# Kernel optimization log

Hardware: AMD Instinct MI355X
Metric: run time of the kernel (lower is better)

The kernel has to match this reference:

```python
import jax, jax.numpy as jnp
import numpy as np

H = 20  # hidden_size

def _lstm_layer(x_tbf, w_ih, w_hh, b_ih, b_hh):
    # x_tbf: [T, B, F]; torch gate order: i, f, g, o
    T, B, _ = x_tbf.shape
    # precompute input projections once: [T, B, 4H]
    xproj = jnp.einsum('tbf,gf->tbg', x_tbf, w_ih) + b_ih + b_hh

    def step(carry, xp_t):
        h, c = carry
        gates = xp_t + h @ w_hh.T  # [B, 4H]
        i, f, g, o = jnp.split(gates, 4, axis=-1)
        i = jax.nn.sigmoid(i)
        f = jax.nn.sigmoid(f)
        g = jnp.tanh(g)
        o = jax.nn.sigmoid(o)
        c = f * c + i * g
        h = o * jnp.tanh(c)
        return (h, c), h

    h0 = jnp.zeros((B, H), dtype=x_tbf.dtype)
    c0 = jnp.zeros((B, H), dtype=x_tbf.dtype)
    (_, _), hs = jax.lax.scan(step, (h0, c0), xproj)
    return hs  # [T, B, H]

def setup_inputs() -> dict:
    key = jax.random.key(0)
    ks = jax.random.split(key, 11)
    F_in = 10
    s_ih0 = 1.0 / np.sqrt(H)
    inp = {
        'x': jax.random.normal(ks[0], (4096, 512, F_in), dtype=jnp.float32),
        'w_ih0': jax.random.uniform(ks[1], (4 * H, F_in), minval=-s_ih0, maxval=s_ih0),
        'w_hh0': jax.random.uniform(ks[2], (4 * H, H), minval=-s_ih0, maxval=s_ih0),
        'b_ih0': jax.random.uniform(ks[3], (4 * H,), minval=-s_ih0, maxval=s_ih0),
        'b_hh0': jax.random.uniform(ks[4], (4 * H,), minval=-s_ih0, maxval=s_ih0),
        'w_ih1': jax.random.uniform(ks[5], (4 * H, H), minval=-s_ih0, maxval=s_ih0),
        'w_hh1': jax.random.uniform(ks[6], (4 * H, H), minval=-s_ih0, maxval=s_ih0),
        'b_ih1': jax.random.uniform(ks[7], (4 * H,), minval=-s_ih0, maxval=s_ih0),
        'b_hh1': jax.random.uniform(ks[8], (4 * H,), minval=-s_ih0, maxval=s_ih0),
        'w_fc': jax.random.uniform(ks[9], (1, H), minval=-s_ih0, maxval=s_ih0),
        'b_fc': jax.random.uniform(ks[10], (1,), minval=-s_ih0, maxval=s_ih0),
    }
    return inp

def reference(x, w_ih0, w_hh0, b_ih0, b_hh0, w_ih1, w_hh1, b_ih1, b_hh1, w_fc, b_fc):
    # x: [B, T, F] (batch_first) -> [T, B, F] for scan
    x_tbf = jnp.swapaxes(x, 0, 1)
    h1 = _lstm_layer(x_tbf, w_ih0, w_hh0, b_ih0, b_hh0)  # [T, B, H]
    h2 = _lstm_layer(h1, w_ih1, w_hh1, b_ih1, b_hh1)     # [T, B, H]
    last = h2[-1]                                          # [B, H]
    return last @ w_fc.T + b_fc                            # [B, 1]
```

## Files before the change

### kernel.cpp

```cpp
#include <hip/hip_runtime.h>

#define T_STEPS 512
#define HS 20
#define F0 10
#define BPB 6
#define NB_TOT 4096
#define NBLK ((NB_TOT + BPB - 1) / BPB)

__device__ __forceinline__ float sigmoid_fast(float v) {
    return __fdividef(1.f, 1.f + __expf(-v));
}
__device__ __forceinline__ float tanh_fast(float v) {
    return 1.f - __fdividef(2.f, __expf(2.f * v) + 1.f);
}
#define PIN(v) asm volatile("" : "+v"(v))

__global__ __launch_bounds__(256, 3)
void lstm2_fc_kernel(const float* __restrict__ x,
                     const float* __restrict__ wih0, const float* __restrict__ whh0,
                     const float* __restrict__ bih0, const float* __restrict__ bhh0,
                     const float* __restrict__ wih1, const float* __restrict__ whh1,
                     const float* __restrict__ bih1, const float* __restrict__ bhh1,
                     const float* __restrict__ wfc,  const float* __restrict__ bfc,
                     float* __restrict__ out)
{
    const int tid   = threadIdx.x;
    const int wid   = tid >> 6;
    const int lane  = tid & 63;
    const int g     = (lane / HS) % 3;
    const int u     = lane % HS;
    const int layer = wid >> 1;
    const int half  = wid & 1;
    const int q0    = 2 * half;
    const int bgA   = blockIdx.x * BPB + g;
    const int bgBr  = blockIdx.x * BPB + g + 3;
    const bool okB  = (bgBr < NB_TOT);
    const int bgB   = okB ? bgBr : (NB_TOT - 1);

    __shared__ float s_h0[2][BPB][HS];
    __shared__ float s_h1[2][BPB][HS];
    __shared__ float ex0[BPB][HS][2];
    __shared__ float ex1[BPB][HS][2];

    for (int i = tid; i < 2 * BPB * HS; i += 256) {
        (&s_h0[0][0][0])[i] = 0.f;
        (&s_h1[0][0][0])[i] = 0.f;
    }

    float w[2][2 * HS], bias[2];
    if (layer == 0) {
        #pragma unroll
        for (int qh = 0; qh < 2; ++qh) {
            const int row = (q0 + qh) * HS + u;
            #pragma unroll
            for (int f = 0; f < F0; ++f) { w[qh][f] = wih0[row * F0 + f]; PIN(w[qh][f]); }
            #pragma unroll
            for (int j = 0; j < HS; ++j) { w[qh][F0 + j] = whh0[row * HS + j]; PIN(w[qh][F0 + j]); }
            bias[qh] = bih0[row] + bhh0[row]; PIN(bias[qh]);
        }
    } else {
        #pragma unroll
        for (int qh = 0; qh < 2; ++qh) {
            const int row = (q0 + qh) * HS + u;
            #pragma unroll
            for (int j = 0; j < HS; ++j) { w[qh][j]      = wih1[row * HS + j]; PIN(w[qh][j]); }
            #pragma unroll
            for (int j = 0; j < HS; ++j) { w[qh][HS + j] = whh1[row * HS + j]; PIN(w[qh][HS + j]); }
            bias[qh] = bih1[row] + bhh1[row]; PIN(bias[qh]);
        }
    }

    float cA = 0.f, cB = 0.f;
    const float* xbA = x + (size_t)bgA * (T_STEPS * F0);
    const float* xbB = x + (size_t)bgB * (T_STEPS * F0);

    float2 xnA[F0 / 2], xnB[F0 / 2];
    if (layer == 0) {
        const float2* pA = (const float2*)xbA;
        const float2* pB = (const float2*)xbB;
        #pragma unroll
        for (int f2 = 0; f2 < F0 / 2; ++f2) { xnA[f2] = pA[f2]; xnB[f2] = pB[f2]; }
    }

    __syncthreads();

    float tgA = 0.f, soA = 0.f, tgB = 0.f, soB = 0.f;

    #pragma unroll 1
    for (int t = 0; t <= T_STEPS; ++t) {
        if (layer == 0) {
            if (t < T_STEPS) {
                float a0A = bias[0], a1A = bias[1];
                float a0B = bias[0], a1B = bias[1];
                #pragma unroll
                for (int f2 = 0; f2 < F0 / 2; ++f2) {
                    const int f = 2 * f2;
                    const float2 vA = xnA[f2], vB = xnB[f2];
                    a0A = fmaf(vA.x, w[0][f], a0A); a0A = fmaf(vA.y, w[0][f + 1], a0A);
                    a1A = fmaf(vA.x, w[1][f], a1A); a1A = fmaf(vA.y, w[1][f + 1], a1A);
                    a0B = fmaf(vB.x, w[0][f], a0B); a0B = fmaf(vB.y, w[0][f + 1], a0B);
                    a1B = fmaf(vB.x, w[1][f], a1B); a1B = fmaf(vB.y, w[1][f + 1], a1B);
                }
                {
                    const int tn = (t + 1 < T_STEPS) ? (t + 1) : (T_STEPS - 1);
                    const float2* pA = (const float2*)(xbA + tn * F0);
                    const float2* pB = (const float2*)(xbB + tn * F0);
                    #pragma unroll
                    for (int f2 = 0; f2 < F0 / 2; ++f2) { xnA[f2] = pA[f2]; xnB[f2] = pB[f2]; }
                }
                const float* hpA = &s_h0[(t + 1) & 1][g][0];
                const float* hpB = &s_h0[(t + 1) & 1][g + 3][0];
                #pragma unroll
                for (int q4 = 0; q4 < HS / 4; ++q4) {
                    const float4 hA = *(const float4*)(hpA + 4 * q4);
                    const float4 hB = *(const float4*)(hpB + 4 * q4);
                    const float eA[4] = {hA.x, hA.y, hA.z, hA.w};
                    const float eB[4] = {hB.x, hB.y, hB.z, hB.w};
                    #pragma unroll
                    for (int e = 0; e < 4; ++e) {
                        const int k = F0 + 4 * q4 + e;
                        a0A = fmaf(eA[e], w[0][k], a0A);  a0B = fmaf(eB[e], w[0][k], a0B);
                        a1A = fmaf(eA[e], w[1][k], a1A);  a1B = fmaf(eB[e], w[1][k], a1B);
                    }
                }
                if (half == 0) {
                    *(float2*)&ex0[g][u][0]     = make_float2(sigmoid_fast(a0A), sigmoid_fast(a1A));
                    *(float2*)&ex0[g + 3][u][0] = make_float2(sigmoid_fast(a0B), sigmoid_fast(a1B));
                } else {
                    tgA = tanh_fast(a0A); soA = sigmoid_fast(a1A);
                    tgB = tanh_fast(a0B); soB = sigmoid_fast(a1B);
                }
            }
        } else {
            if (t >= 1) {
                float a0A = bias[0], a1A = bias[1];
                float a0B = bias[0], a1B = bias[1];
                const float* hpA = &s_h0[(t - 1) & 1][g][0];
                const float* hpB = &s_h0[(t - 1) & 1][g + 3][0];
                #pragma unroll
                for (int q4 = 0; q4 < HS / 4; ++q4) {
                    const float4 hA = *(const float4*)(hpA + 4 * q4);
                    const float4 hB = *(const float4*)(hpB + 4 * q4);
                    const float eA[4] = {hA.x, hA.y, hA.z, hA.w};
                    const float eB[4] = {hB.x, hB.y, hB.z, hB.w};
                    #pragma unroll
                    for (int e = 0; e < 4; ++e) {
                        const int k = 4 * q4 + e;
                        a0A = fmaf(eA[e], w[0][k], a0A);  a0B = fmaf(eB[e], w[0][k], a0B);
                        a1A = fmaf(eA[e], w[1][k], a1A);  a1B = fmaf(eB[e], w[1][k], a1B);
                    }
                }
                const float* ppA = &s_h1[t & 1][g][0];
                const float* ppB = &s_h1[t & 1][g + 3][0];
                #pragma unroll
                for (int q4 = 0; q4 < HS / 4; ++q4) {
                    const float4 hA = *(const float4*)(ppA + 4 * q4);
                    const float4 hB = *(const float4*)(ppB + 4 * q4);
                    const float eA[4] = {hA.x, hA.y, hA.z, hA.w};
                    const float eB[4] = {hB.x, hB.y, hB.z, hB.w};
                    #pragma unroll
                    for (int e = 0; e < 4; ++e) {
                        const int k = HS + 4 * q4 + e;
                        a0A = fmaf(eA[e], w[0][k], a0A);  a0B = fmaf(eB[e], w[0][k], a0B);
                        a1A = fmaf(eA[e], w[1][k], a1A);  a1B = fmaf(eB[e], w[1][k], a1B);
                    }
                }
                if (half == 0) {
                    *(float2*)&ex1[g][u][0]     = make_float2(sigmoid_fast(a0A), sigmoid_fast(a1A));
                    *(float2*)&ex1[g + 3][u][0] = make_float2(sigmoid_fast(a0B), sigmoid_fast(a1B));
                } else {
                    tgA = tanh_fast(a0A); soA = sigmoid_fast(a1A);
                    tgB = tanh_fast(a0B); soB = sigmoid_fast(a1B);
                }
            }
        }
        __syncthreads();

        if (half == 1) {
            const bool act = (layer == 0) ? (t < T_STEPS) : (t >= 1);
            if (act) {
                float2 sifA, sifB;
                if (layer == 0) {
                    sifA = *(const float2*)&ex0[g][u][0];
                    sifB = *(const float2*)&ex0[g + 3][u][0];
                } else {
                    sifA = *(const float2*)&ex1[g][u][0];
                    sifB = *(const float2*)&ex1[g + 3][u][0];
                }
                cA = fmaf(sifA.y, cA, sifA.x * tgA);
                cB = fmaf(sifB.y, cB, sifB.x * tgB);
                const float hA = soA * tanh_fast(cA);
                const float hB = soB * tanh_fast(cB);
                if (layer == 0) {
                    s_h0[t & 1][g][u]       = hA;
                    s_h0[t & 1][g + 3][u]   = hB;
                } else {
                    s_h1[(t - 1) & 1][g][u]     = hA;
                    s_h1[(t - 1) & 1][g + 3][u] = hB;
                }
            }
        }
        __syncthreads();
    }

    if (wid == 3 && lane < 60 && u == 0) {
        const int sl = (T_STEPS - 1) & 1;
        float oA = bfc[0], oB = bfc[0];
        #pragma unroll
        for (int j = 0; j < HS; ++j) {
            oA = fmaf(s_h1[sl][g][j],     wfc[j], oA);
            oB = fmaf(s_h1[sl][g + 3][j], wfc[j], oB);
        }
        out[bgA] = oA;
        if (okB) out[bgBr] = oB;
    }
}

extern "C" void kernel_launch(void* const* d_in, const int* in_sizes, int n_in,
                              void* d_out, int out_size, void* d_ws, size_t ws_size,
                              hipStream_t stream) {
    const float* x    = (const float*)d_in[0];
    const float* wih0 = (const float*)d_in[1];
    const float* whh0 = (const float*)d_in[2];
    const float* bih0 = (const float*)d_in[3];
    const float* bhh0 = (const float*)d_in[4];
    const float* wih1 = (const float*)d_in[5];
    const float* whh1 = (const float*)d_in[6];
    const float* bih1 = (const float*)d_in[7];
    const float* bhh1 = (const float*)d_in[8];
    const float* wfc  = (const float*)d_in[9];
    const float* bfc  = (const float*)d_in[10];
    float* out = (float*)d_out;

    dim3 grid(NBLK), block(256);
    hipLaunchKernelGGL(lstm2_fc_kernel, grid, block, 0, stream,
                       x, wih0, whh0, bih0, bhh0,
                       wih1, whh1, bih1, bhh1, wfc, bfc, out);
}
```

Before: 749.5 us.

## Split gates across eight waves and pipeline cell update to drop one barrier

Doubles the block to 512 threads so each wave computes a single gate (i, f, g, o) instead of two, halving per-thread FMA work and weight registers. Gate activations go to double-buffered shared memory, and every wave applies the cell/hidden update for the previous step at the start of the next iteration. This removes the second __syncthreads per timestep, at the cost of a longer pipeline (T+3 iterations) and redundant cell updates across the four gate waves. Occupancy bounds change to 512 threads with 6 blocks requested.

New measurement: 1.553 ms. 107% more time.

```diff
diff --git a/kernel.cpp b/kernel.cpp
--- a/kernel.cpp
+++ b/kernel.cpp
@@ -15,7 +15,7 @@
 }
 #define PIN(v) asm volatile("" : "+v"(v))
 
-__global__ __launch_bounds__(256, 3)
+__global__ __launch_bounds__(512, 6)
 void lstm2_fc_kernel(const float* __restrict__ x,
                      const float* __restrict__ wih0, const float* __restrict__ whh0,
                      const float* __restrict__ bih0, const float* __restrict__ bhh0,
@@ -29,9 +29,8 @@
     const int lane  = tid & 63;
     const int g     = (lane / HS) % 3;
     const int u     = lane % HS;
-    const int layer = wid >> 1;
-    const int half  = wid & 1;
-    const int q0    = 2 * half;
+    const int layer = wid >> 2;
+    const int q     = wid & 3;
     const int bgA   = blockIdx.x * BPB + g;
     const int bgBr  = blockIdx.x * BPB + g + 3;
     const bool okB  = (bgBr < NB_TOT);
@@ -39,34 +38,29 @@
 
     __shared__ float s_h0[2][BPB][HS];
     __shared__ float s_h1[2][BPB][HS];
-    __shared__ float ex0[BPB][HS][2];
-    __shared__ float ex1[BPB][HS][2];
-
-    for (int i = tid; i < 2 * BPB * HS; i += 256) {
+    __shared__ float ex0[2][BPB][HS][4];
+    __shared__ float ex1[2][BPB][HS][4];
+
+    for (int i = tid; i < 2 * BPB * HS; i += 512) {
         (&s_h0[0][0][0])[i] = 0.f;
         (&s_h1[0][0][0])[i] = 0.f;
     }
 
-    float w[2][2 * HS], bias[2];
-    if (layer == 0) {
-        #pragma unroll
-        for (int qh = 0; qh < 2; ++qh) {
-            const int row = (q0 + qh) * HS + u;
-            #pragma unroll
-            for (int f = 0; f < F0; ++f) { w[qh][f] = wih0[row * F0 + f]; PIN(w[qh][f]); }
-            #pragma unroll
-            for (int j = 0; j < HS; ++j) { w[qh][F0 + j] = whh0[row * HS + j]; PIN(w[qh][F0 + j]); }
-            bias[qh] = bih0[row] + bhh0[row]; PIN(bias[qh]);
-        }
-    } else {
-        #pragma unroll
-        for (int qh = 0; qh < 2; ++qh) {
-            const int row = (q0 + qh) * HS + u;
-            #pragma unroll
-            for (int j = 0; j < HS; ++j) { w[qh][j]      = wih1[row * HS + j]; PIN(w[qh][j]); }
-            #pragma unroll
-            for (int j = 0; j < HS; ++j) { w[qh][HS + j] = whh1[row * HS + j]; PIN(w[qh][HS + j]); }
-            bias[qh] = bih1[row] + bhh1[row]; PIN(bias[qh]);
+    float w[2 * HS], bias;
+    {
+        const int row = q * HS + u;
+        if (layer == 0) {
+            #pragma unroll
+            for (int f = 0; f < F0; ++f) { w[f] = wih0[row * F0 + f]; PIN(w[f]); }
+            #pragma unroll
+            for (int j = 0; j < HS; ++j) { w[F0 + j] = whh0[row * HS + j]; PIN(w[F0 + j]); }
+            bias = bih0[row] + bhh0[row]; PIN(bias);
+        } else {
+            #pragma unroll
+            for (int j = 0; j < HS; ++j) { w[j]      = wih1[row * HS + j]; PIN(w[j]); }
+            #pragma unroll
+            for (int j = 0; j < HS; ++j) { w[HS + j] = whh1[row * HS + j]; PIN(w[HS + j]); }
+            bias = bih1[row] + bhh1[row]; PIN(bias);
         }
     }
 
@@ -84,22 +78,26 @@
 
     __syncthreads();
 
-    float tgA = 0.f, soA = 0.f, tgB = 0.f, soB = 0.f;
-
     #pragma unroll 1
-    for (int t = 0; t <= T_STEPS; ++t) {
+    for (int t = 0; t < T_STEPS + 3; ++t) {
         if (layer == 0) {
+            if (t >= 1 && t <= T_STEPS) {
+                const int sl = (t - 1) & 1;
+                const float4 eA = *(const float4*)&ex0[sl][g][u][0];
+                const float4 eB = *(const float4*)&ex0[sl][g + 3][u][0];
+                cA = fmaf(eA.y, cA, eA.x * eA.z);
+                cB = fmaf(eB.y, cB, eB.x * eB.z);
+                s_h0[sl][g][u]     = eA.w * tanh_fast(cA);
+                s_h0[sl][g + 3][u] = eB.w * tanh_fast(cB);
+            }
             if (t < T_STEPS) {
-                float a0A = bias[0], a1A = bias[1];
-                float a0B = bias[0], a1B = bias[1];
+                float aA = bias, aB = bias;
                 #pragma unroll
                 for (int f2 = 0; f2 < F0 / 2; ++f2) {
                     const int f = 2 * f2;
                     const float2 vA = xnA[f2], vB = xnB[f2];
-                    a0A = fmaf(vA.x, w[0][f], a0A); a0A = fmaf(vA.y, w[0][f + 1], a0A);
-                    a1A = fmaf(vA.x, w[1][f], a1A); a1A = fmaf(vA.y, w[1][f + 1], a1A);
-                    a0B = fmaf(vB.x, w[0][f], a0B); a0B = fmaf(vB.y, w[0][f + 1], a0B);
-                    a1B = fmaf(vB.x, w[1][f], a1B); a1B = fmaf(vB.y, w[1][f + 1], a1B);
+                    aA = fmaf(vA.x, w[f], aA); aA = fmaf(vA.y, w[f + 1], aA);
+                    aB = fmaf(vB.x, w[f], aB); aB = fmaf(vB.y, w[f + 1], aB);
                 }
                 {
                     const int tn = (t + 1 < T_STEPS) ? (t + 1) : (T_STEPS - 1);
@@ -108,8 +106,9 @@
                     #pragma unroll
                     for (int f2 = 0; f2 < F0 / 2; ++f2) { xnA[f2] = pA[f2]; xnB[f2] = pB[f2]; }
                 }
-                const float* hpA = &s_h0[(t + 1) & 1][g][0];
-                const float* hpB = &s_h0[(t + 1) & 1][g + 3][0];
+                const int sl = (t + 1) & 1;
+                const float* hpA = &s_h0[sl][g][0];
+                const float* hpB = &s_h0[sl][g + 3][0];
                 #pragma unroll
                 for (int q4 = 0; q4 < HS / 4; ++q4) {
                     const float4 hA = *(const float4*)(hpA + 4 * q4);
@@ -119,24 +118,31 @@
                     #pragma unroll
                     for (int e = 0; e < 4; ++e) {
                         const int k = F0 + 4 * q4 + e;
-                        a0A = fmaf(eA[e], w[0][k], a0A);  a0B = fmaf(eB[e], w[0][k], a0B);
-                        a1A = fmaf(eA[e], w[1][k], a1A);  a1B = fmaf(eB[e], w[1][k], a1B);
+                        aA = fmaf(eA[e], w[k], aA);
+                        aB = fmaf(eB[e], w[k], aB);
                     }
                 }
-                if (half == 0) {
-                    *(float2*)&ex0[g][u][0]     = make_float2(sigmoid_fast(a0A), sigmoid_fast(a1A));
-                    *(float2*)&ex0[g + 3][u][0] = make_float2(sigmoid_fast(a0B), sigmoid_fast(a1B));
-                } else {
-                    tgA = tanh_fast(a0A); soA = sigmoid_fast(a1A);
-                    tgB = tanh_fast(a0B); soB = sigmoid_fast(a1B);
-                }
+                float actA, actB;
+                if (q == 2) { actA = tanh_fast(aA);    actB = tanh_fast(aB); }
+                else        { actA = sigmoid_fast(aA); actB = sigmoid_fast(aB); }
+                ex0[t & 1][g][u][q]     = actA;
+                ex0[t & 1][g + 3][u][q] = actB;
             }
         } else {
-            if (t >= 1) {
-                float a0A = bias[0], a1A = bias[1];
-                float a0B = bias[0], a1B = bias[1];
-                const float* hpA = &s_h0[(t - 1) & 1][g][0];
-                const float* hpB = &s_h0[(t - 1) & 1][g + 3][0];
+            if (t >= 3) {
+                const int sl = (t - 3) & 1;
+                const float4 eA = *(const float4*)&ex1[sl][g][u][0];
+                const float4 eB = *(const float4*)&ex1[sl][g + 3][u][0];
+                cA = fmaf(eA.y, cA, eA.x * eA.z);
+                cB = fmaf(eB.y, cB, eB.x * eB.z);
+                s_h1[sl][g][u]     = eA.w * tanh_fast(cA);
+                s_h1[sl][g + 3][u] = eB.w * tanh_fast(cB);
+            }
+            if (t >= 2 && t < T_STEPS + 2) {
+                float aA = bias, aB = bias;
+                const int sl0 = t & 1;
+                const float* hpA = &s_h0[sl0][g][0];
+                const float* hpB = &s_h0[sl0][g + 3][0];
                 #pragma unroll
                 for (int q4 = 0; q4 < HS / 4; ++q4) {
                     const float4 hA = *(const float4*)(hpA + 4 * q4);
@@ -146,12 +152,13 @@
                     #pragma unroll
                     for (int e = 0; e < 4; ++e) {
                         const int k = 4 * q4 + e;
-                        a0A = fmaf(eA[e], w[0][k], a0A);  a0B = fmaf(eB[e], w[0][k], a0B);
-                        a1A = fmaf(eA[e], w[1][k], a1A);  a1B = fmaf(eB[e], w[1][k], a1B);
+                        aA = fmaf(eA[e], w[k], aA);
+                        aB = fmaf(eB[e], w[k], aB);
                     }
                 }
-                const float* ppA = &s_h1[t & 1][g][0];
-                const float* ppB = &s_h1[t & 1][g + 3][0];
+                const int sl1 = (t + 1) & 1;
+                const float* ppA = &s_h1[sl1][g][0];
+                const float* ppB = &s_h1[sl1][g + 3][0];
                 #pragma unroll
                 for (int q4 = 0; q4 < HS / 4; ++q4) {
                     const float4 hA = *(const float4*)(ppA + 4 * q4);
@@ -161,49 +168,21 @@
                     #pragma unroll
                     for (int e = 0; e < 4; ++e) {
                         const int k = HS + 4 * q4 + e;
-                        a0A = fmaf(eA[e], w[0][k], a0A);  a0B = fmaf(eB[e], w[0][k], a0B);
-                        a1A = fmaf(eA[e], w[1][k], a1A);  a1B = fmaf(eB[e], w[1][k], a1B);
+                        aA = fmaf(eA[e], w[k], aA);
+                        aB = fmaf(eB[e], w[k], aB);
                     }
                 }
-                if (half == 0) {
-                    *(float2*)&ex1[g][u][0]     = make_float2(sigmoid_fast(a0A), sigmoid_fast(a1A));
-                    *(float2*)&ex1[g + 3][u][0] = make_float2(sigmoid_fast(a0B), sigmoid_fast(a1B));
-                } else {
-                    tgA = tanh_fast(a0A); soA = sigmoid_fast(a1A);
-                    tgB = tanh_fast(a0B); soB = sigmoid_fast(a1B);
-                }
+                float actA, actB;
+                if (q == 2) { actA = tanh_fast(aA);    actB = tanh_fast(aB); }
+                else        { actA = sigmoid_fast(aA); actB = sigmoid_fast(aB); }
+                ex1[t & 1][g][u][q]     = actA;
+                ex1[t & 1][g + 3][u][q] = actB;
             }
         }
         __syncthreads();
-
-        if (half == 1) {
-            const bool act = (layer == 0) ? (t < T_STEPS) : (t >= 1);
-            if (act) {
-                float2 sifA, sifB;
-                if (layer == 0) {
-                    sifA = *(const float2*)&ex0[g][u][0];
-                    sifB = *(const float2*)&ex0[g + 3][u][0];
-                } else {
-                    sifA = *(const float2*)&ex1[g][u][0];
-                    sifB = *(const float2*)&ex1[g + 3][u][0];
-                }
-                cA = fmaf(sifA.y, cA, sifA.x * tgA);
-                cB = fmaf(sifB.y, cB, sifB.x * tgB);
-                const float hA = soA * tanh_fast(cA);
-                const float hB = soB * tanh_fast(cB);
-                if (layer == 0) {
-                    s_h0[t & 1][g][u]       = hA;
-                    s_h0[t & 1][g + 3][u]   = hB;
-                } else {
-                    s_h1[(t - 1) & 1][g][u]     = hA;
-                    s_h1[(t - 1) & 1][g + 3][u] = hB;
-                }
-            }
-        }
-        __syncthreads();
-    }
-
-    if (wid == 3 && lane < 60 && u == 0) {
+    }
+
+    if (wid == 7 && lane < 60 && u == 0) {
         const int sl = (T_STEPS - 1) & 1;
         float oA = bfc[0], oB = bfc[0];
         #pragma unroll
@@ -232,7 +211,7 @@
     const float* bfc  = (const float*)d_in[10];
     float* out = (float*)d_out;
 
-    dim3 grid(NBLK), block(256);
+    dim3 grid(NBLK), block(512);
     hipLaunchKernelGGL(lstm2_fc_kernel, grid, block, 0, stream,
                        x, wih0, whh0, bih0, bhh0,
                        wih1, whh1, bih1, bhh1, wfc, bfc, out);
```

## Pipeline cell update one step behind to halve barriers; stage x chunks in LDS

Applied to the files above, without the earlier changes.

The cell/hidden-state update is moved into the next iteration so each timestep needs one __syncthreads instead of two. Both halves now write activations into a double-buffered exchange array, and layer 1 is skewed by extra steps. Input x is loaded cooperatively in 16-step chunks into double-buffered shared memory instead of per-thread strided global loads each step. This lengthens the pipeline by a few iterations, uses more LDS, and makes the all-waves elementwise update redundant across the two halves.

Result: slower. 849.8 us (+13.4%).

```diff
diff --git a/kernel.cpp b/kernel.cpp
--- a/kernel.cpp
+++ b/kernel.cpp
@@ -6,6 +6,9 @@
 #define BPB 6
 #define NB_TOT 4096
 #define NBLK ((NB_TOT + BPB - 1) / BPB)
+#define CHK 16
+#define NCH (T_STEPS / CHK)
+#define XCHW (CHK * BPB * F0)
 
 __device__ __forceinline__ float sigmoid_fast(float v) {
     return __fdividef(1.f, 1.f + __expf(-v));
@@ -14,6 +17,17 @@
     return 1.f - __fdividef(2.f, __expf(2.f * v) + 1.f);
 }
 #define PIN(v) asm volatile("" : "+v"(v))
+
+__device__ __forceinline__ float stage_ld(const float* __restrict__ x,
+                                          int bx, int cc, int i) {
+    const int s = i / (BPB * F0);
+    const int r = i - s * (BPB * F0);
+    const int b = r / F0;
+    const int f = r - b * F0;
+    int gb = bx * BPB + b; gb = (gb < NB_TOT) ? gb : (NB_TOT - 1);
+    int ts = cc * CHK + s; ts = (ts < T_STEPS) ? ts : (T_STEPS - 1);
+    return x[(size_t)gb * (T_STEPS * F0) + ts * F0 + f];
+}
 
 __global__ __launch_bounds__(256, 3)
 void lstm2_fc_kernel(const float* __restrict__ x,
@@ -32,15 +46,22 @@
     const int layer = wid >> 1;
     const int half  = wid & 1;
     const int q0    = 2 * half;
-    const int bgA   = blockIdx.x * BPB + g;
-    const int bgBr  = blockIdx.x * BPB + g + 3;
+    const int bx    = blockIdx.x;
+    const int bgA   = bx * BPB + g;
+    const int bgBr  = bx * BPB + g + 3;
     const bool okB  = (bgBr < NB_TOT);
-    const int bgB   = okB ? bgBr : (NB_TOT - 1);
 
     __shared__ float s_h0[2][BPB][HS];
     __shared__ float s_h1[2][BPB][HS];
-    __shared__ float ex0[BPB][HS][2];
-    __shared__ float ex1[BPB][HS][2];
+    __shared__ float ex0[2][BPB][HS][4];
+    __shared__ float ex1[2][BPB][HS][4];
+    __shared__ float xs[2][XCHW];
+
+    const int i3c = (tid + 768 < XCHW) ? (tid + 768) : (XCHW - 1);
+    float sv0 = stage_ld(x, bx, 0, tid);
+    float sv1 = stage_ld(x, bx, 0, tid + 256);
+    float sv2 = stage_ld(x, bx, 0, tid + 512);
+    float sv3 = stage_ld(x, bx, 0, i3c);
 
     for (int i = tid; i < 2 * BPB * HS; i += 256) {
         (&s_h0[0][0][0])[i] = 0.f;
@@ -71,42 +92,49 @@
     }
 
     float cA = 0.f, cB = 0.f;
-    const float* xbA = x + (size_t)bgA * (T_STEPS * F0);
-    const float* xbB = x + (size_t)bgB * (T_STEPS * F0);
-
-    float2 xnA[F0 / 2], xnB[F0 / 2];
-    if (layer == 0) {
-        const float2* pA = (const float2*)xbA;
-        const float2* pB = (const float2*)xbB;
-        #pragma unroll
-        for (int f2 = 0; f2 < F0 / 2; ++f2) { xnA[f2] = pA[f2]; xnB[f2] = pB[f2]; }
-    }
-
+
+    xs[0][tid]       = sv0;
+    xs[0][tid + 256] = sv1;
+    xs[0][tid + 512] = sv2;
+    xs[0][i3c]       = sv3;
     __syncthreads();
 
-    float tgA = 0.f, soA = 0.f, tgB = 0.f, soB = 0.f;
-
     #pragma unroll 1
-    for (int t = 0; t <= T_STEPS; ++t) {
+    for (int t = 0; t < T_STEPS + 3; ++t) {
+        const bool do_stage = ((t & (CHK - 1)) == 0) && (((t >> 4) + 1) < NCH);
+        const int scc = (t >> 4) + 1;
+        float tv0, tv1, tv2, tv3;
+        if (do_stage) {
+            tv0 = stage_ld(x, bx, scc, tid);
+            tv1 = stage_ld(x, bx, scc, tid + 256);
+            tv2 = stage_ld(x, bx, scc, tid + 512);
+            tv3 = stage_ld(x, bx, scc, i3c);
+        }
+
         if (layer == 0) {
+            if (t >= 1 && t <= T_STEPS) {
+                const int sl = (t - 1) & 1;
+                const float4 eA = *(const float4*)&ex0[sl][g][u][0];
+                const float4 eB = *(const float4*)&ex0[sl][g + 3][u][0];
+                cA = fmaf(eA.y, cA, eA.x * eA.z);
+                cB = fmaf(eB.y, cB, eB.x * eB.z);
+                s_h0[sl][g][u]     = eA.w * tanh_fast(cA);
+                s_h0[sl][g + 3][u] = eB.w * tanh_fast(cB);
+            }
             if (t < T_STEPS) {
                 float a0A = bias[0], a1A = bias[1];
                 float a0B = bias[0], a1B = bias[1];
+                const float* xr = &xs[(t >> 4) & 1][(t & (CHK - 1)) * (BPB * F0)];
+                const float2* xpA = (const float2*)(xr + g * F0);
+                const float2* xpB = (const float2*)(xr + (g + 3) * F0);
                 #pragma unroll
                 for (int f2 = 0; f2 < F0 / 2; ++f2) {
                     const int f = 2 * f2;
-                    const float2 vA = xnA[f2], vB = xnB[f2];
+                    const float2 vA = xpA[f2], vB = xpB[f2];
                     a0A = fmaf(vA.x, w[0][f], a0A); a0A = fmaf(vA.y, w[0][f + 1], a0A);
                     a1A = fmaf(vA.x, w[1][f], a1A); a1A = fmaf(vA.y, w[1][f + 1], a1A);
                     a0B = fmaf(vB.x, w[0][f], a0B); a0B = fmaf(vB.y, w[0][f + 1], a0B);
                     a1B = fmaf(vB.x, w[1][f], a1B); a1B = fmaf(vB.y, w[1][f + 1], a1B);
-                }
-                {
-                    const int tn = (t + 1 < T_STEPS) ? (t + 1) : (T_STEPS - 1);
-                    const float2* pA = (const float2*)(xbA + tn * F0);
-                    const float2* pB = (const float2*)(xbB + tn * F0);
-                    #pragma unroll
-                    for (int f2 = 0; f2 < F0 / 2; ++f2) { xnA[f2] = pA[f2]; xnB[f2] = pB[f2]; }
                 }
                 const float* hpA = &s_h0[(t + 1) & 1][g][0];
                 const float* hpB = &s_h0[(t + 1) & 1][g + 3][0];
@@ -123,20 +151,32 @@
                         a1A = fmaf(eA[e], w[1][k], a1A);  a1B = fmaf(eB[e], w[1][k], a1B);
                     }
                 }
+                float act0A, act1A, act0B, act1B;
                 if (half == 0) {
-                    *(float2*)&ex0[g][u][0]     = make_float2(sigmoid_fast(a0A), sigmoid_fast(a1A));
-                    *(float2*)&ex0[g + 3][u][0] = make_float2(sigmoid_fast(a0B), sigmoid_fast(a1B));
+                    act0A = sigmoid_fast(a0A); act1A = sigmoid_fast(a1A);
+                    act0B = sigmoid_fast(a0B); act1B = sigmoid_fast(a1B);
                 } else {
-                    tgA = tanh_fast(a0A); soA = sigmoid_fast(a1A);
-                    tgB = tanh_fast(a0B); soB = sigmoid_fast(a1B);
-                }
+                    act0A = tanh_fast(a0A);    act1A = sigmoid_fast(a1A);
+                    act0B = tanh_fast(a0B);    act1B = sigmoid_fast(a1B);
+                }
+                *(float2*)&ex0[t & 1][g][u][q0]     = make_float2(act0A, act1A);
+                *(float2*)&ex0[t & 1][g + 3][u][q0] = make_float2(act0B, act1B);
             }
         } else {
-            if (t >= 1) {
+            if (t >= 3) {
+                const int sl = (t - 3) & 1;
+                const float4 eA = *(const float4*)&ex1[sl][g][u][0];
+                const float4 eB = *(const float4*)&ex1[sl][g + 3][u][0];
+                cA = fmaf(eA.y, cA, eA.x * eA.z);
+                cB = fmaf(eB.y, cB, eB.x * eB.z);
+                s_h1[sl][g][u]     = eA.w * tanh_fast(cA);
+                s_h1[sl][g + 3][u] = eB.w * tanh_fast(cB);
+            }
+            if (t >= 2 && t < T_STEPS + 2) {
                 float a0A = bias[0], a1A = bias[1];
                 float a0B = bias[0], a1B = bias[1];
-                const float* hpA = &s_h0[(t - 1) & 1][g][0];
-                const float* hpB = &s_h0[(t - 1) & 1][g + 3][0];
+                const float* hpA = &s_h0[t & 1][g][0];
+                const float* hpB = &s_h0[t & 1][g + 3][0];
                 #pragma unroll
                 for (int q4 = 0; q4 < HS / 4; ++q4) {
                     const float4 hA = *(const float4*)(hpA + 4 * q4);
@@ -150,8 +190,8 @@
                         a1A = fmaf(eA[e], w[1][k], a1A);  a1B = fmaf(eB[e], w[1][k], a1B);
                     }
                 }
-                const float* ppA = &s_h1[t & 1][g][0];
-                const float* ppB = &s_h1[t & 1][g + 3][0];
+                const float* ppA = &s_h1[(t + 1) & 1][g][0];
+                const float* ppB = &s_h1[(t + 1) & 1][g + 3][0];
                 #pragma unroll
                 for (int q4 = 0; q4 < HS / 4; ++q4) {
                     const float4 hA = *(const float4*)(ppA + 4 * q4);
@@ -165,40 +205,25 @@
                         a1A = fmaf(eA[e], w[1][k], a1A);  a1B = fmaf(eB[e], w[1][k], a1B);
                     }
                 }
+                float act0A, act1A, act0B, act1B;
                 if (half == 0) {
-                    *(float2*)&ex1[g][u][0]     = make_float2(sigmoid_fast(a0A), sigmoid_fast(a1A));
-                    *(float2*)&ex1[g + 3][u][0] = make_float2(sigmoid_fast(a0B), sigmoid_fast(a1B));
+                    act0A = sigmoid_fast(a0A); act1A = sigmoid_fast(a1A);
+                    act0B = sigmoid_fast(a0B); act1B = sigmoid_fast(a1B);
                 } else {
-                    tgA = tanh_fast(a0A); soA = sigmoid_fast(a1A);
-                    tgB = tanh_fast(a0B); soB = sigmoid_fast(a1B);
-                }
-            }
-        }
-        __syncthreads();
-
-        if (half == 1) {
-            const bool act = (layer == 0) ? (t < T_STEPS) : (t >= 1);
-            if (act) {
-                float2 sifA, sifB;
-                if (layer == 0) {
-                    sifA = *(const float2*)&ex0[g][u][0];
-                    sifB = *(const float2*)&ex0[g + 3][u][0];
-                } else {
-                    sifA = *(const float2*)&ex1[g][u][0];
-                    sifB = *(const float2*)&ex1[g + 3][u][0];
-                }
-                cA = fmaf(sifA.y, cA, sifA.x * tgA);
-                cB = fmaf(sifB.y, cB, sifB.x * tgB);
-                const float hA = soA * tanh_fast(cA);
-                const float hB = soB * tanh_fast(cB);
-                if (layer == 0) {
-                    s_h0[t & 1][g][u]       = hA;
-                    s_h0[t & 1][g + 3][u]   = hB;
-                } else {
-                    s_h1[(t - 1) & 1][g][u]     = hA;
-                    s_h1[(t - 1) & 1][g + 3][u] = hB;
-                }
-            }
+                    act0A = tanh_fast(a0A);    act1A = sigmoid_fast(a1A);
+                    act0B = tanh_fast(a0B);    act1B = sigmoid_fast(a1B);
+                }
+                *(float2*)&ex1[t & 1][g][u][q0]     = make_float2(act0A, act1A);
+                *(float2*)&ex1[t & 1][g + 3][u][q0] = make_float2(act0B, act1B);
+            }
+        }
+
+        if (do_stage) {
+            float* xw = &xs[scc & 1][0];
+            xw[tid]       = tv0;
+            xw[tid + 256] = tv1;
+            xw[tid + 512] = tv2;
+            xw[i3c]       = tv3;
         }
         __syncthreads();
     }
```

## Replace block-wide barriers with per-wave LDS flag handshakes between LSTM stages

Applied to the files above, without the earlier changes.

Drops the two __syncthreads per timestep and gives each of the four waves its own loop, which signals progress through monotonically increasing counters in shared memory, spin-waiting with s_sleep. The layer-0 h buffer goes to four slots and the gate exchange buffers are double-buffered, so layer 0 can run ahead of layer 1 and the two halves of each layer synchronise only pairwise. The aim is to remove barrier stalls and let the two layers pipeline. In exchange it relies on volatile LDS polling and fences for correctness, and sleeping waves may add latency.

After: 2.732 ms. +264.5%, slower.

```diff
diff --git a/kernel.cpp b/kernel.cpp
--- a/kernel.cpp
+++ b/kernel.cpp
@@ -14,6 +14,15 @@
     return 1.f - __fdividef(2.f, __expf(2.f * v) + 1.f);
 }
 #define PIN(v) asm volatile("" : "+v"(v))
+
+__device__ __forceinline__ void waitflag(const volatile int* f, int tgt) {
+    while (*f < tgt) __builtin_amdgcn_s_sleep(1);
+    asm volatile("" ::: "memory");
+}
+__device__ __forceinline__ void pubflag(volatile int* f, int v, int lane) {
+    __threadfence_block();
+    if (lane == 0) *f = v;
+}
 
 __global__ __launch_bounds__(256, 3)
 void lstm2_fc_kernel(const float* __restrict__ x,
@@ -37,15 +46,15 @@
     const bool okB  = (bgBr < NB_TOT);
     const int bgB   = okB ? bgBr : (NB_TOT - 1);
 
-    __shared__ float s_h0[2][BPB][HS];
+    __shared__ float s_h0[4][BPB][HS];
     __shared__ float s_h1[2][BPB][HS];
-    __shared__ float ex0[BPB][HS][2];
-    __shared__ float ex1[BPB][HS][2];
-
-    for (int i = tid; i < 2 * BPB * HS; i += 256) {
-        (&s_h0[0][0][0])[i] = 0.f;
-        (&s_h1[0][0][0])[i] = 0.f;
-    }
+    __shared__ float ex0[2][BPB][HS][2];
+    __shared__ float ex1[2][BPB][HS][2];
+    __shared__ int   flg[6];
+
+    for (int i = tid; i < 4 * BPB * HS; i += 256) (&s_h0[0][0][0])[i] = 0.f;
+    for (int i = tid; i < 2 * BPB * HS; i += 256) (&s_h1[0][0][0])[i] = 0.f;
+    if (tid < 6) flg[tid] = 0;
 
     float w[2][2 * HS], bias[2];
     if (layer == 0) {
@@ -84,135 +93,197 @@
 
     __syncthreads();
 
-    float tgA = 0.f, soA = 0.f, tgB = 0.f, soB = 0.f;
-
-    #pragma unroll 1
-    for (int t = 0; t <= T_STEPS; ++t) {
-        if (layer == 0) {
-            if (t < T_STEPS) {
-                float a0A = bias[0], a1A = bias[1];
-                float a0B = bias[0], a1B = bias[1];
-                #pragma unroll
-                for (int f2 = 0; f2 < F0 / 2; ++f2) {
-                    const int f = 2 * f2;
-                    const float2 vA = xnA[f2], vB = xnB[f2];
-                    a0A = fmaf(vA.x, w[0][f], a0A); a0A = fmaf(vA.y, w[0][f + 1], a0A);
-                    a1A = fmaf(vA.x, w[1][f], a1A); a1A = fmaf(vA.y, w[1][f + 1], a1A);
-                    a0B = fmaf(vB.x, w[0][f], a0B); a0B = fmaf(vB.y, w[0][f + 1], a0B);
-                    a1B = fmaf(vB.x, w[1][f], a1B); a1B = fmaf(vB.y, w[1][f + 1], a1B);
-                }
-                {
-                    const int tn = (t + 1 < T_STEPS) ? (t + 1) : (T_STEPS - 1);
-                    const float2* pA = (const float2*)(xbA + tn * F0);
-                    const float2* pB = (const float2*)(xbB + tn * F0);
-                    #pragma unroll
-                    for (int f2 = 0; f2 < F0 / 2; ++f2) { xnA[f2] = pA[f2]; xnB[f2] = pB[f2]; }
-                }
-                const float* hpA = &s_h0[(t + 1) & 1][g][0];
-                const float* hpB = &s_h0[(t + 1) & 1][g + 3][0];
-                #pragma unroll
-                for (int q4 = 0; q4 < HS / 4; ++q4) {
-                    const float4 hA = *(const float4*)(hpA + 4 * q4);
-                    const float4 hB = *(const float4*)(hpB + 4 * q4);
-                    const float eA[4] = {hA.x, hA.y, hA.z, hA.w};
-                    const float eB[4] = {hB.x, hB.y, hB.z, hB.w};
-                    #pragma unroll
-                    for (int e = 0; e < 4; ++e) {
-                        const int k = F0 + 4 * q4 + e;
-                        a0A = fmaf(eA[e], w[0][k], a0A);  a0B = fmaf(eB[e], w[0][k], a0B);
-                        a1A = fmaf(eA[e], w[1][k], a1A);  a1B = fmaf(eB[e], w[1][k], a1B);
-                    }
-                }
-                if (half == 0) {
-                    *(float2*)&ex0[g][u][0]     = make_float2(sigmoid_fast(a0A), sigmoid_fast(a1A));
-                    *(float2*)&ex0[g + 3][u][0] = make_float2(sigmoid_fast(a0B), sigmoid_fast(a1B));
-                } else {
-                    tgA = tanh_fast(a0A); soA = sigmoid_fast(a1A);
-                    tgB = tanh_fast(a0B); soB = sigmoid_fast(a1B);
-                }
-            }
-        } else {
-            if (t >= 1) {
-                float a0A = bias[0], a1A = bias[1];
-                float a0B = bias[0], a1B = bias[1];
-                const float* hpA = &s_h0[(t - 1) & 1][g][0];
-                const float* hpB = &s_h0[(t - 1) & 1][g + 3][0];
-                #pragma unroll
-                for (int q4 = 0; q4 < HS / 4; ++q4) {
-                    const float4 hA = *(const float4*)(hpA + 4 * q4);
-                    const float4 hB = *(const float4*)(hpB + 4 * q4);
-                    const float eA[4] = {hA.x, hA.y, hA.z, hA.w};
-                    const float eB[4] = {hB.x, hB.y, hB.z, hB.w};
-                    #pragma unroll
-                    for (int e = 0; e < 4; ++e) {
-                        const int k = 4 * q4 + e;
-                        a0A = fmaf(eA[e], w[0][k], a0A);  a0B = fmaf(eB[e], w[0][k], a0B);
-                        a1A = fmaf(eA[e], w[1][k], a1A);  a1B = fmaf(eB[e], w[1][k], a1B);
-                    }
-                }
-                const float* ppA = &s_h1[t & 1][g][0];
-                const float* ppB = &s_h1[t & 1][g + 3][0];
-                #pragma unroll
-                for (int q4 = 0; q4 < HS / 4; ++q4) {
-                    const float4 hA = *(const float4*)(ppA + 4 * q4);
-                    const float4 hB = *(const float4*)(ppB + 4 * q4);
-                    const float eA[4] = {hA.x, hA.y, hA.z, hA.w};
-                    const float eB[4] = {hB.x, hB.y, hB.z, hB.w};
-                    #pragma unroll
-                    for (int e = 0; e < 4; ++e) {
-                        const int k = HS + 4 * q4 + e;
-                        a0A = fmaf(eA[e], w[0][k], a0A);  a0B = fmaf(eB[e], w[0][k], a0B);
-                        a1A = fmaf(eA[e], w[1][k], a1A);  a1B = fmaf(eB[e], w[1][k], a1B);
-                    }
-                }
-                if (half == 0) {
-                    *(float2*)&ex1[g][u][0]     = make_float2(sigmoid_fast(a0A), sigmoid_fast(a1A));
-                    *(float2*)&ex1[g + 3][u][0] = make_float2(sigmoid_fast(a0B), sigmoid_fast(a1B));
-                } else {
-                    tgA = tanh_fast(a0A); soA = sigmoid_fast(a1A);
-                    tgB = tanh_fast(a0B); soB = sigmoid_fast(a1B);
-                }
-            }
-        }
-        __syncthreads();
-
-        if (half == 1) {
-            const bool act = (layer == 0) ? (t < T_STEPS) : (t >= 1);
-            if (act) {
-                float2 sifA, sifB;
-                if (layer == 0) {
-                    sifA = *(const float2*)&ex0[g][u][0];
-                    sifB = *(const float2*)&ex0[g + 3][u][0];
-                } else {
-                    sifA = *(const float2*)&ex1[g][u][0];
-                    sifB = *(const float2*)&ex1[g + 3][u][0];
-                }
-                cA = fmaf(sifA.y, cA, sifA.x * tgA);
-                cB = fmaf(sifB.y, cB, sifB.x * tgB);
-                const float hA = soA * tanh_fast(cA);
-                const float hB = soB * tanh_fast(cB);
-                if (layer == 0) {
-                    s_h0[t & 1][g][u]       = hA;
-                    s_h0[t & 1][g + 3][u]   = hB;
-                } else {
-                    s_h1[(t - 1) & 1][g][u]     = hA;
-                    s_h1[(t - 1) & 1][g + 3][u] = hB;
-                }
-            }
-        }
-        __syncthreads();
-    }
-
-    if (wid == 3 && lane < 60 && u == 0) {
-        const int sl = (T_STEPS - 1) & 1;
-        float oA = bfc[0], oB = bfc[0];
-        #pragma unroll
-        for (int j = 0; j < HS; ++j) {
-            oA = fmaf(s_h1[sl][g][j],     wfc[j], oA);
-            oB = fmaf(s_h1[sl][g + 3][j], wfc[j], oB);
-        }
-        out[bgA] = oA;
-        if (okB) out[bgBr] = oB;
+    if (wid == 0) {
+        #pragma unroll 1
+        for (int t = 0; t < T_STEPS; ++t) {
+            float a0A = bias[0], a1A = bias[1], a0B = bias[0], a1B = bias[1];
+            #pragma unroll
+            for (int f2 = 0; f2 < F0 / 2; ++f2) {
+                const int f = 2 * f2;
+                const float2 vA = xnA[f2], vB = xnB[f2];
+                a0A = fmaf(vA.x, w[0][f], a0A); a0A = fmaf(vA.y, w[0][f + 1], a0A);
+                a1A = fmaf(vA.x, w[1][f], a1A); a1A = fmaf(vA.y, w[1][f + 1], a1A);
+                a0B = fmaf(vB.x, w[0][f], a0B); a0B = fmaf(vB.y, w[0][f + 1], a0B);
+                a1B = fmaf(vB.x, w[1][f], a1B); a1B = fmaf(vB.y, w[1][f + 1], a1B);
+            }
+            {
+                const int tn = (t + 1 < T_STEPS) ? (t + 1) : (T_STEPS - 1);
+                const float2* pA = (const float2*)(xbA + tn * F0);
+                const float2* pB = (const float2*)(xbB + tn * F0);
+                #pragma unroll
+                for (int f2 = 0; f2 < F0 / 2; ++f2) { xnA[f2] = pA[f2]; xnB[f2] = pB[f2]; }
+            }
+            waitflag(&flg[1], t);
+            const float* hpA = &s_h0[(t - 1) & 3][g][0];
+            const float* hpB = &s_h0[(t - 1) & 3][g + 3][0];
+            #pragma unroll
+            for (int q4 = 0; q4 < HS / 4; ++q4) {
+                const float4 hA = *(const float4*)(hpA + 4 * q4);
+                const float4 hB = *(const float4*)(hpB + 4 * q4);
+                const float eA[4] = {hA.x, hA.y, hA.z, hA.w};
+                const float eB[4] = {hB.x, hB.y, hB.z, hB.w};
+                #pragma unroll
+                for (int e = 0; e < 4; ++e) {
+                    const int k = F0 + 4 * q4 + e;
+                    a0A = fmaf(eA[e], w[0][k], a0A);  a0B = fmaf(eB[e], w[0][k], a0B);
+                    a1A = fmaf(eA[e], w[1][k], a1A);  a1B = fmaf(eB[e], w[1][k], a1B);
+                }
+            }
+            *(float2*)&ex0[t & 1][g][u][0]     = make_float2(sigmoid_fast(a0A), sigmoid_fast(a1A));
+            *(float2*)&ex0[t & 1][g + 3][u][0] = make_float2(sigmoid_fast(a0B), sigmoid_fast(a1B));
+            pubflag(&flg[0], t + 1, lane);
+        }
+    } else if (wid == 1) {
+        #pragma unroll 1
+        for (int t = 0; t < T_STEPS; ++t) {
+            float a0A = bias[0], a1A = bias[1], a0B = bias[0], a1B = bias[1];
+            #pragma unroll
+            for (int f2 = 0; f2 < F0 / 2; ++f2) {
+                const int f = 2 * f2;
+                const float2 vA = xnA[f2], vB = xnB[f2];
+                a0A = fmaf(vA.x, w[0][f], a0A); a0A = fmaf(vA.y, w[0][f + 1], a0A);
+                a1A = fmaf(vA.x, w[1][f], a1A); a1A = fmaf(vA.y, w[1][f + 1], a1A);
+                a0B = fmaf(vB.x, w[0][f], a0B); a0B = fmaf(vB.y, w[0][f + 1], a0B);
+                a1B = fmaf(vB.x, w[1][f], a1B); a1B = fmaf(vB.y, w[1][f + 1], a1B);
+            }
+            {
+                const int tn = (t + 1 < T_STEPS) ? (t + 1) : (T_STEPS - 1);
+                const float2* pA = (const float2*)(xbA + tn * F0);
+                const float2* pB = (const float2*)(xbB + tn * F0);
+                #pragma unroll
+                for (int f2 = 0; f2 < F0 / 2; ++f2) { xnA[f2] = pA[f2]; xnB[f2] = pB[f2]; }
+            }
+            const float* hpA = &s_h0[(t - 1) & 3][g][0];
+            const float* hpB = &s_h0[(t - 1) & 3][g + 3][0];
+            #pragma unroll
+            for (int q4 = 0; q4 < HS / 4; ++q4) {
+                const float4 hA = *(const float4*)(hpA + 4 * q4);
+                const float4 hB = *(const float4*)(hpB + 4 * q4);
+                const float eA[4] = {hA.x, hA.y, hA.z, hA.w};
+                const float eB[4] = {hB.x, hB.y, hB.z, hB.w};
+                #pragma unroll
+                for (int e = 0; e < 4; ++e) {
+                    const int k = F0 + 4 * q4 + e;
+                    a0A = fmaf(eA[e], w[0][k], a0A);  a0B = fmaf(eB[e], w[0][k], a0B);
+                    a1A = fmaf(eA[e], w[1][k], a1A);  a1B = fmaf(eB[e], w[1][k], a1B);
+                }
+            }
+            const float tgA = tanh_fast(a0A), soA = sigmoid_fast(a1A);
+            const float tgB = tanh_fast(a0B), soB = sigmoid_fast(a1B);
+            waitflag(&flg[0], t + 1);
+            const float2 sifA = *(const float2*)&ex0[t & 1][g][u][0];
+            const float2 sifB = *(const float2*)&ex0[t & 1][g + 3][u][0];
+            cA = fmaf(sifA.y, cA, sifA.x * tgA);
+            cB = fmaf(sifB.y, cB, sifB.x * tgB);
+            const float hA = soA * tanh_fast(cA);
+            const float hB = soB * tanh_fast(cB);
+            waitflag(&flg[4], t - 3);
+            waitflag(&flg[5], t - 3);
+            s_h0[t & 3][g][u]     = hA;
+            s_h0[t & 3][g + 3][u] = hB;
+            pubflag(&flg[1], t + 1, lane);
+        }
+    } else if (wid == 2) {
+        #pragma unroll 1
+        for (int s = 0; s < T_STEPS; ++s) {
+            float a0A = bias[0], a1A = bias[1], a0B = bias[0], a1B = bias[1];
+            waitflag(&flg[1], s + 1);
+            const float* hpA = &s_h0[s & 3][g][0];
+            const float* hpB = &s_h0[s & 3][g + 3][0];
+            #pragma unroll
+            for (int q4 = 0; q4 < HS / 4; ++q4) {
+                const float4 hA = *(const float4*)(hpA + 4 * q4);
+                const float4 hB = *(const float4*)(hpB + 4 * q4);
+                const float eA[4] = {hA.x, hA.y, hA.z, hA.w};
+                const float eB[4] = {hB.x, hB.y, hB.z, hB.w};
+                #pragma unroll
+                for (int e = 0; e < 4; ++e) {
+                    const int k = 4 * q4 + e;
+                    a0A = fmaf(eA[e], w[0][k], a0A);  a0B = fmaf(eB[e], w[0][k], a0B);
+                    a1A = fmaf(eA[e], w[1][k], a1A);  a1B = fmaf(eB[e], w[1][k], a1B);
+                }
+            }
+            pubflag(&flg[4], s + 1, lane);
+            waitflag(&flg[3], s);
+            const float* ppA = &s_h1[(s - 1) & 1][g][0];
+            const float* ppB = &s_h1[(s - 1) & 1][g + 3][0];
+            #pragma unroll
+            for (int q4 = 0; q4 < HS / 4; ++q4) {
+                const float4 hA = *(const float4*)(ppA + 4 * q4);
+                const float4 hB = *(const float4*)(ppB + 4 * q4);
+                const float eA[4] = {hA.x, hA.y, hA.z, hA.w};
+                const float eB[4] = {hB.x, hB.y, hB.z, hB.w};
+                #pragma unroll
+                for (int e = 0; e < 4; ++e) {
+                    const int k = HS + 4 * q4 + e;
+                    a0A = fmaf(eA[e], w[0][k], a0A);  a0B = fmaf(eB[e], w[0][k], a0B);
+                    a1A = fmaf(eA[e], w[1][k], a1A);  a1B = fmaf(eB[e], w[1][k], a1B);
+                }
+            }
+            *(float2*)&ex1[s & 1][g][u][0]     = make_float2(sigmoid_fast(a0A), sigmoid_fast(a1A));
+            *(float2*)&ex1[s & 1][g + 3][u][0] = make_float2(sigmoid_fast(a0B), sigmoid_fast(a1B));
+            pubflag(&flg[2], s + 1, lane);
+        }
+    } else {
+        #pragma unroll 1
+        for (int s = 0; s < T_STEPS; ++s) {
+            float a0A = bias[0], a1A = bias[1], a0B = bias[0], a1B = bias[1];
+            waitflag(&flg[1], s + 1);
+            const float* hpA = &s_h0[s & 3][g][0];
+            const float* hpB = &s_h0[s & 3][g + 3][0];
+            #pragma unroll
+            for (int q4 = 0; q4 < HS / 4; ++q4) {
+                const float4 hA = *(const float4*)(hpA + 4 * q4);
+                const float4 hB = *(const float4*)(hpB + 4 * q4);
+                const float eA[4] = {hA.x, hA.y, hA.z, hA.w};
+                const float eB[4] = {hB.x, hB.y, hB.z, hB.w};
+                #pragma unroll
+                for (int e = 0; e < 4; ++e) {
+                    const int k = 4 * q4 + e;
+                    a0A = fmaf(eA[e], w[0][k], a0A);  a0B = fmaf(eB[e], w[0][k], a0B);
+                    a1A = fmaf(eA[e], w[1][k], a1A);  a1B = fmaf(eB[e], w[1][k], a1B);
+                }
+            }
+            pubflag(&flg[5], s + 1, lane);
+            const float* ppA = &s_h1[(s - 1) & 1][g][0];
+            const float* ppB = &s_h1[(s - 1) & 1][g + 3][0];
+            #pragma unroll
+            for (int q4 = 0; q4 < HS / 4; ++q4) {
+                const float4 hA = *(const float4*)(ppA + 4 * q4);
+                const float4 hB = *(const float4*)(ppB + 4 * q4);
+                const float eA[4] = {hA.x, hA.y, hA.z, hA.w};
+                const float eB[4] = {hB.x, hB.y, hB.z, hB.w};
+                #pragma unroll
+                for (int e = 0; e < 4; ++e) {
+                    const int k = HS + 4 * q4 + e;
+                    a0A = fmaf(eA[e], w[0][k], a0A);  a0B = fmaf(eB[e], w[0][k], a0B);
+                    a1A = fmaf(eA[e], w[1][k], a1A);  a1B = fmaf(eB[e], w[1][k], a1B);
+                }
+            }
+            const float tgA = tanh_fast(a0A), soA = sigmoid_fast(a1A);
+            const float tgB = tanh_fast(a0B), soB = sigmoid_fast(a1B);
+            waitflag(&flg[2], s + 1);
+            const float2 sifA = *(const float2*)&ex1[s & 1][g][u][0];
+            const float2 sifB = *(const float2*)&ex1[s & 1][g + 3][u][0];
+            cA = fmaf(sifA.y, cA, sifA.x * tgA);
+            cB = fmaf(sifB.y, cB, sifB.x * tgB);
+            const float hA = soA * tanh_fast(cA);
+            const float hB = soB * tanh_fast(cB);
+            s_h1[s & 1][g][u]     = hA;
+            s_h1[s & 1][g + 3][u] = hB;
+            pubflag(&flg[3], s + 1, lane);
+        }
+        if (lane < 60 && u == 0) {
+            const int sl = (T_STEPS - 1) & 1;
+            float oA = bfc[0], oB = bfc[0];
+            #pragma unroll
+            for (int j = 0; j < HS; ++j) {
+                oA = fmaf(s_h1[sl][g][j],     wfc[j], oA);
+                oB = fmaf(s_h1[sl][g + 3][j], wfc[j], oB);
+            }
+            out[bgA] = oA;
+            if (okB) out[bgBr] = oB;
+        }
     }
 }
 
```
